# Kernel optimization log

Hardware: AMD Instinct MI355X
Metric: run time of the kernel (lower is better)

Reference implementation:

```python
import jax, jax.numpy as jnp
import numpy as np

SH_C0 = 0.28209479177387814  # degree-0 SH basis constant (3DGS convention)
LOWPASS = 0.3                # 2D covariance dilation used by the 3DGS rasterizer
NEAR_CULL = 0.2              # view-space z cull threshold in the CUDA kernel


def _render(extrinsics, intrinsics, near, far, h, w, bg, means, covs, shs, opac):
    B, G, _ = means.shape
    # ---- scale-invariant normalization (scale = 1/near) ----
    scale = 1.0 / near                                        # [B]
    extr = extrinsics.at[:, :3, 3].multiply(scale[:, None])
    covs = covs * (scale ** 2)[:, None, None, None]
    means = means * scale[:, None, None]
    near = near * scale

    view = jnp.linalg.inv(extr)                               # world -> camera
    R, t = view[:, :3, :3], view[:, :3, 3]
    cam = jnp.einsum('bij,bgj->bgi', R, means) + t[:, None, :]  # [B,G,3] view-space
    tz = cam[..., 2]

    fx, fy = intrinsics[:, 0, 0], intrinsics[:, 1, 1]
    cx, cy = intrinsics[:, 0, 2], intrinsics[:, 1, 2]
    fx_p, fy_p = fx * w, fy * h                               # focal in pixels
    cx_p, cy_p = cx * w, cy * h
    lim_x = (1.3 * (0.5 / fx))[:, None]                       # tan(fov/2) clamps (EWA)
    lim_y = (1.3 * (0.5 / fy))[:, None]

    # ---- EWA splatting: project 3D covariance to 2D conic ----
    txz = jnp.clip(cam[..., 0] / tz, -lim_x, lim_x) * tz
    tyz = jnp.clip(cam[..., 1] / tz, -lim_y, lim_y) * tz
    zero = jnp.zeros_like(tz)
    J = jnp.stack([
        jnp.stack([fx_p[:, None] / tz, zero, -fx_p[:, None] * txz / (tz * tz)], axis=-1),
        jnp.stack([zero, fy_p[:, None] / tz, -fy_p[:, None] * tyz / (tz * tz)], axis=-1),
    ], axis=-2)                                               # [B,G,2,3]
    M = jnp.einsum('bgij,bjk->bgik', J, R)                    # [B,G,2,3]
    cov2d = jnp.einsum('bgij,bgjk,bglk->bgil', M, covs, M)    # [B,G,2,2]
    a = cov2d[..., 0, 0] + LOWPASS
    bb = cov2d[..., 0, 1]
    c = cov2d[..., 1, 1] + LOWPASS
    det = a * c - bb * bb
    inv_det = jnp.where(det != 0, 1.0 / det, 0.0)
    conA, conB, conC = c * inv_det, -bb * inv_det, a * inv_det

    # ---- projected 2D means in pixel coords (ndc2pix) ----
    mx = fx_p[:, None] * cam[..., 0] / tz + cx_p[:, None] - 0.5
    my = fy_p[:, None] * cam[..., 1] / tz + cy_p[:, None] - 0.5

    # degree-0 SH -> RGB (clamped to >= 0 as in the kernel)
    colors = jnp.maximum(SH_C0 * shs[..., 0] + 0.5, 0.0)      # [B,G,3]

    # ---- global front-to-back depth sort per batch ----
    valid = (tz > NEAR_CULL) & (det > 0)
    order = jnp.argsort(jnp.where(valid, tz, jnp.inf), axis=1)
    take = lambda x: jnp.take_along_axis(x, order, axis=1)
    mx, my = take(mx), take(my)
    conA, conB, conC = take(conA), take(conB), take(conC)
    tzs, valid, op = take(tz), take(valid), take(opac)
    colors = jnp.take_along_axis(colors, order[..., None], axis=1)

    # ---- per-pixel alpha compositing ----
    px = jnp.tile(jnp.arange(w, dtype=jnp.float32), h)        # [HW]
    py = jnp.repeat(jnp.arange(h, dtype=jnp.float32), w)
    dx = px[None, None, :] - mx[..., None]                    # [B,G,HW]
    dy = py[None, None, :] - my[..., None]
    power = -0.5 * (conA[..., None] * dx * dx + conC[..., None] * dy * dy) \
            - conB[..., None] * dx * dy
    alpha = jnp.minimum(0.99, op[..., None] * jnp.exp(power))
    alpha = jnp.where((power <= 0) & (alpha >= 1.0 / 255.0) & valid[..., None], alpha, 0.0)
    Tcum = jnp.cumprod(1.0 - alpha, axis=1)                   # [B,G,HW]
    T_excl = jnp.concatenate([jnp.ones_like(Tcum[:, :1]), Tcum[:, :-1]], axis=1)
    wgt = alpha * T_excl                                      # contribution weights
    T_fin = Tcum[:, -1]                                       # [B,HW]

    img = jnp.einsum('bgp,bgc->bcp', wgt, colors) + T_fin[:, None, :] * bg[:, :, None]
    depth = jnp.sum(wgt * tzs[..., None], axis=1)
    op_map = jnp.sum(wgt, axis=1)
    return (img.reshape(B, 3, h, w), depth.reshape(B, h, w), op_map.reshape(B, 1, h, w))


def setup_inputs() -> dict:
    key = jax.random.key(0)
    ks = jax.random.split(key, 6)
    B, G, H, W = 2, 1024, 128, 128
    extr = jnp.tile(jnp.eye(4, dtype=jnp.float32)[None], (B, 1, 1))
    extr = extr.at[:, :3, 3].set(0.05 * jax.random.normal(ks[0], (B, 3), dtype=jnp.float32))
    intr = jnp.tile(jnp.array([[1.0, 0.0, 0.5], [0.0, 1.0, 0.5], [0.0, 0.0, 1.0]],
                              dtype=jnp.float32)[None], (B, 1, 1))
    near = jnp.ones((B,), jnp.float32)
    far = jnp.full((B,), 100.0, jnp.float32)
    bg = jnp.zeros((B, 3), jnp.float32)
    xy = jax.random.normal(ks[1], (B, G, 2), dtype=jnp.float32)
    zc = jax.random.uniform(ks[2], (B, G, 1), minval=2.0, maxval=6.0, dtype=jnp.float32)
    means = jnp.concatenate([xy, zc], axis=-1)
    L = 0.02 * jax.random.normal(ks[3], (B, G, 3, 3), dtype=jnp.float32)
    covs = jnp.einsum('bgij,bgkj->bgik', L, L) + 1e-4 * jnp.eye(3, dtype=jnp.float32)
    shs = 0.5 * jax.random.normal(ks[4], (B, G, 3, 1), dtype=jnp.float32)
    op = jax.random.uniform(ks[5], (B, G), dtype=jnp.float32)
    return {"extrinsics": extr, "intrinsics": intr, "near": near, "far": far,
            "h": H, "w": W, "background_color": bg, "gaussian_means": means,
            "gaussian_covariances": covs, "gaussian_sh_coefficients": shs,
            "gaussian_opacities": op}


def reference(extrinsics, intrinsics, near, far, h, w, background_color,
              gaussian_means, gaussian_covariances, gaussian_sh_coefficients,
              gaussian_opacities):
    return _render(extrinsics, intrinsics, near, far, h, w, background_color,
                   gaussian_means, gaussian_covariances, gaussian_sh_coefficients,
                   gaussian_opacities)
```

## Files before the change

### kernel.cpp

```cpp
#include <hip/hip_runtime.h>
#include <math.h>

#define SMAX 1024
#define EPS_T 1e-4f


__global__ __launch_bounds__(256) void prep_kernel(
    const float* __restrict__ extr,
    const float* __restrict__ intr,
    const float* __restrict__ nearv,
    const int* __restrict__ hp,
    const int* __restrict__ wp,
    const float* __restrict__ means,
    const float* __restrict__ covs,
    const float* __restrict__ shs,
    const float* __restrict__ opac,
    float* __restrict__ ws,
    int B, int G)
{
  const int i = blockIdx.x * blockDim.x + threadIdx.x;
  const int BG = B * G;
  if (i >= BG) return;
  const int b = i / G;

  const float hf = (float)hp[0];
  const float wf = (float)wp[0];
  const float scale = 1.0f / nearv[b];
  const float s2 = scale * scale;

  const float* E = extr + b * 16;
  const float A00=E[0], A01=E[1], A02=E[2];
  const float A10=E[4], A11=E[5], A12=E[6];
  const float A20=E[8], A21=E[9], A22=E[10];
  const float te0=E[3]*scale, te1=E[7]*scale, te2=E[11]*scale;
  const float co00 =  (A11*A22 - A12*A21);
  const float co10 = -(A10*A22 - A12*A20);
  const float co20 =  (A10*A21 - A11*A20);
  const float idA = 1.0f / (A00*co00 + A01*co10 + A02*co20);
  const float R00 = co00*idA;
  const float R01 = -(A01*A22 - A02*A21)*idA;
  const float R02 =  (A01*A12 - A02*A11)*idA;
  const float R10 = co10*idA;
  const float R11 =  (A00*A22 - A02*A20)*idA;
  const float R12 = -(A00*A12 - A02*A10)*idA;
  const float R20 = co20*idA;
  const float R21 = -(A00*A21 - A01*A20)*idA;
  const float R22 =  (A00*A11 - A01*A10)*idA;
  const float t0 = -(R00*te0 + R01*te1 + R02*te2);
  const float t1 = -(R10*te0 + R11*te1 + R12*te2);
  const float t2 = -(R20*te0 + R21*te1 + R22*te2);

  const float fx = intr[b*9+0], fy = intr[b*9+4];
  const float cx = intr[b*9+2], cy = intr[b*9+5];
  const float fx_p = fx*wf, fy_p = fy*hf, cx_p = cx*wf, cy_p = cy*hf;
  const float lim_x = 1.3f*0.5f/fx, lim_y = 1.3f*0.5f/fy;

  const float* mp = means + (size_t)i*3;
  float m0 = mp[0]*scale, m1 = mp[1]*scale, m2 = mp[2]*scale;
  float camx = R00*m0 + R01*m1 + R02*m2 + t0;
  float camy = R10*m0 + R11*m1 + R12*m2 + t1;
  float tz   = R20*m0 + R21*m1 + R22*m2 + t2;
  float itz = 1.0f / tz;
  const float* Cp = covs + (size_t)i*9;
  float C00=Cp[0]*s2, C01=Cp[1]*s2, C02=Cp[2]*s2;
  float C10=Cp[3]*s2, C11=Cp[4]*s2, C12=Cp[5]*s2;
  float C20=Cp[6]*s2, C21=Cp[7]*s2, C22=Cp[8]*s2;
  float txz = fminf(fmaxf(camx*itz, -lim_x), lim_x) * tz;
  float tyz = fminf(fmaxf(camy*itz, -lim_y), lim_y) * tz;
  float j00 = fx_p*itz, j02 = -fx_p*txz*itz*itz;
  float j11 = fy_p*itz, j12 = -fy_p*tyz*itz*itz;
  float M00 = j00*R00 + j02*R20;
  float M01 = j00*R01 + j02*R21;
  float M02 = j00*R02 + j02*R22;
  float M10 = j11*R10 + j12*R20;
  float M11 = j11*R11 + j12*R21;
  float M12 = j11*R12 + j12*R22;
  float v0 = C00*M00 + C01*M01 + C02*M02;
  float v1 = C10*M00 + C11*M01 + C12*M02;
  float v2 = C20*M00 + C21*M01 + C22*M02;
  float u0 = C00*M10 + C01*M11 + C02*M12;
  float u1 = C10*M10 + C11*M11 + C12*M12;
  float u2 = C20*M10 + C21*M11 + C22*M12;
  float a  = M00*v0 + M01*v1 + M02*v2 + 0.3f;
  float bb = M00*u0 + M01*u1 + M02*u2;
  float c  = M10*u0 + M11*u1 + M12*u2 + 0.3f;
  float det2 = a*c - bb*bb;
  float invd = (det2 != 0.0f) ? (1.0f/det2) : 0.0f;
  float conA = c*invd, conB = -bb*invd, conC = a*invd;
  float mx = fx_p*camx*itz + cx_p - 0.5f;
  float my = fy_p*camy*itz + cy_p - 0.5f;
  float op = opac[i];
  const float* sp = shs + (size_t)i*3;
  float col0 = fmaxf(0.28209479177387814f*sp[0] + 0.5f, 0.0f);
  float col1 = fmaxf(0.28209479177387814f*sp[1] + 0.5f, 0.0f);
  float col2 = fmaxf(0.28209479177387814f*sp[2] + 0.5f, 0.0f);
  float r2max = 2.0f * logf(255.0f * op);
  bool valid = (tz > 0.2f) && (det2 > 0.0f) && (r2max > 0.0f);
  float rx = sqrtf(fmaxf(r2max*a, 0.0f)) + 0.01f;
  float ry = sqrtf(fmaxf(r2max*c, 0.0f)) + 0.01f;

  float4* compv = (float4*)ws;
  compv[(size_t)i*3+0] = make_float4(mx, my, conA, conB);
  compv[(size_t)i*3+1] = make_float4(conC, op, col0, col1);
  compv[(size_t)i*3+2] = make_float4(col2, tz, 0.f, 0.f);
  float4* cullv = (float4*)(ws + (size_t)BG*12);
  cullv[i] = make_float4(valid ? mx : 1e9f, my, rx, ry);
  ws[(size_t)BG*16 + i] = tz;
}

__global__ __launch_bounds__(256) void render_kernel(
    const float* __restrict__ ws,
    const float* __restrict__ bg,
    const int* __restrict__ wp,
    float* __restrict__ out,
    int B, int G, int hw)
{
  const int tid = threadIdx.x;
  const int lane = tid & 63;
  const int wv = tid >> 6;
  const int tiles_per_img = hw >> 8;
  const int b = blockIdx.x / tiles_per_img;
  const int tile = blockIdx.x % tiles_per_img;
  const int w = wp[0];
  const int tiles_x = w >> 4;
  const int tx = tile % tiles_x;
  const int ty = tile / tiles_x;
  const int qx = (wv & 1) << 3;
  const int qy = (wv >> 1) << 3;
  const int px = (tx << 4) + qx + (lane & 7);
  const int py = (ty << 4) + qy + (lane >> 3);
  const float pxf = (float)px, pyf = (float)py;
  const float bx0 = (float)((tx << 4) + qx) - 0.01f;
  const float bx1 = bx0 + 7.02f;
  const float by0 = (float)((ty << 4) + qy) - 0.01f;
  const float by1 = by0 + 7.02f;

  const int BG = B * G;
  const int base = b * G;
  const float4* compv = (const float4*)ws;
  const float4* cullv = (const float4*)(ws + (size_t)BG*12);
  const float*  tza   = ws + (size_t)BG*16;

  __shared__ float  s_key[4][SMAX];
  __shared__ int    s_idx[4][SMAX];
  __shared__ float4 s_c[4][64][3];

  int cnt = 0;
  for (int g0 = 0; g0 < G; g0 += 64) {
    const int g = g0 + lane;
    bool surv = false;
    if (g < G) {
      float4 cu = cullv[base + g];
      surv = (cu.x - cu.z <= bx1) && (cu.x + cu.z >= bx0) &&
             (cu.y - cu.w <= by1) && (cu.y + cu.w >= by0);
    }
    unsigned long long m = __ballot(surv);
    if (surv) {
      int pos = cnt + __popcll(m & ((1ull << lane) - 1ull));
      if (pos < SMAX) {
        s_key[wv][pos] = tza[base + g];
        s_idx[wv][pos] = g;
      }
    }
    cnt += __popcll(m);
  }
  cnt = min(cnt, SMAX);

  float T = 1.0f, a0 = 0.f, a1 = 0.f, a2 = 0.f, da = 0.f, wa = 0.f;

  if (cnt > 0) {
    int n2 = 1;
    while (n2 < cnt) n2 <<= 1;
    for (int i2 = cnt + lane; i2 < n2; i2 += 64) {
      s_key[wv][i2] = INFINITY;
      s_idx[wv][i2] = 0x7fffffff;
    }
    __builtin_amdgcn_wave_barrier();

    for (int k2 = 2; k2 <= n2; k2 <<= 1) {
      for (int j = k2 >> 1; j > 0; j >>= 1) {
        for (int i2 = lane; i2 < n2; i2 += 64) {
          int ixj = i2 ^ j;
          if (ixj > i2) {
            float ki = s_key[wv][i2], kj = s_key[wv][ixj];
            int   ii = s_idx[wv][i2], ij = s_idx[wv][ixj];
            bool up = ((i2 & k2) == 0);
            bool gt = (ki > kj) || (ki == kj && ii > ij);
            if (up ? gt : !gt && !(ki == kj && ii == ij)) {
              s_key[wv][i2] = kj; s_key[wv][ixj] = ki;
              s_idx[wv][i2] = ij; s_idx[wv][ixj] = ii;
            }
          }
        }
        __builtin_amdgcn_wave_barrier();
      }
    }

    for (int c0 = 0; c0 < cnt; c0 += 64) {
      const int mlen = min(64, cnt - c0);
      if (lane < mlen) {
        const int g = s_idx[wv][c0 + lane];
        const float4* cp = compv + (size_t)(base + g) * 3;
        s_c[wv][lane][0] = cp[0];
        s_c[wv][lane][1] = cp[1];
        s_c[wv][lane][2] = cp[2];
      }
      __builtin_amdgcn_wave_barrier();
      for (int i2 = 0; i2 < mlen; i2++) {
        const float4 A  = s_c[wv][i2][0];
        const float4 Bv = s_c[wv][i2][1];
        const float4 Cv = s_c[wv][i2][2];
        const float dx = pxf - A.x;
        const float dy = pyf - A.y;
        const float q = A.z*dx*dx + 2.0f*A.w*dx*dy + Bv.x*dy*dy;
        if (q >= 0.0f && T >= EPS_T) {
          float al = fminf(Bv.y * __expf(-0.5f*q), 0.99f);
          if (al >= (1.0f/255.0f)) {
            const float wgt = al * T;
            a0 += wgt * Bv.z;
            a1 += wgt * Bv.w;
            a2 += wgt * Cv.x;
            da += wgt * Cv.y;
            wa += wgt;
            T *= (1.0f - al);
          }
        }
      }
      if (__ballot(T >= EPS_T) == 0ull) break;
      __builtin_amdgcn_wave_barrier();
    }
  }

  const int pixidx = py * w + px;
  const size_t io = (size_t)b * 3 * hw;
  out[io + 0*(size_t)hw + pixidx] = a0 + T * bg[b*3+0];
  out[io + 1*(size_t)hw + pixidx] = a1 + T * bg[b*3+1];
  out[io + 2*(size_t)hw + pixidx] = a2 + T * bg[b*3+2];
  out[(size_t)B*3*hw + (size_t)b*hw + pixidx] = da;
  out[(size_t)B*4*hw + (size_t)b*hw + pixidx] = wa;
}

extern "C" void kernel_launch(void* const* d_in, const int* in_sizes, int n_in,
                              void* d_out, int out_size, void* d_ws, size_t ws_size,
                              hipStream_t stream) {
  const float* extr  = (const float*)d_in[0];
  const float* intr  = (const float*)d_in[1];
  const float* nearv = (const float*)d_in[2];
  const int*   hp    = (const int*)d_in[4];
  const int*   wp    = (const int*)d_in[5];
  const float* bg    = (const float*)d_in[6];
  const float* means = (const float*)d_in[7];
  const float* covs  = (const float*)d_in[8];
  const float* shs   = (const float*)d_in[9];
  const float* opac  = (const float*)d_in[10];

  const int B  = in_sizes[2];
  const int G  = in_sizes[10] / B;
  const int hw = out_size / (5 * B);

  float* ws  = (float*)d_ws;
  float* out = (float*)d_out;

  const int BG = B * G;
  prep_kernel<<<(BG + 255) / 256, 256, 0, stream>>>(
      extr, intr, nearv, hp, wp, means, covs, shs, opac, ws, B, G);
  const int tiles = hw / 256;
  render_kernel<<<B * tiles, 256, 0, stream>>>(ws, bg, wp, out, B, G, hw);
}
```

Measured before the change: 96.56 us.

## Fuse Gaussian preprocessing into render kernel with shared-memory staging and packed sort keys

Removes the separate preprocessing kernel. Each render block now recomputes projection, conic and color for all Gaussians of its image into shared memory, and culling and compositing read from there instead of a global workspace. The depth-sort uses packed 64-bit (depth, index) keys, which halves shared-memory traffic per compare-exchange. The early-exit ballot now runs every 32 Gaussians. The costs are redundant per-block preprocessing, a hard G_MAX=1024 limit, and a per-wave sort capacity reduced from 1024 to 256, which could truncate lists.

Result: no change. 94.91 us (-1.7%).

```diff
diff --git a/kernel.cpp b/kernel.cpp
--- a/kernel.cpp
+++ b/kernel.cpp
@@ -1,117 +1,22 @@
 #include <hip/hip_runtime.h>
 #include <math.h>
 
-#define SMAX 1024
+#define G_MAX 1024
+#define SMAX 256
 #define EPS_T 1e-4f
 
 
-__global__ __launch_bounds__(256) void prep_kernel(
+__global__ __launch_bounds__(256) void render_all(
     const float* __restrict__ extr,
     const float* __restrict__ intr,
     const float* __restrict__ nearv,
     const int* __restrict__ hp,
     const int* __restrict__ wp,
+    const float* __restrict__ bg,
     const float* __restrict__ means,
     const float* __restrict__ covs,
     const float* __restrict__ shs,
     const float* __restrict__ opac,
-    float* __restrict__ ws,
-    int B, int G)
-{
-  const int i = blockIdx.x * blockDim.x + threadIdx.x;
-  const int BG = B * G;
-  if (i >= BG) return;
-  const int b = i / G;
-
-  const float hf = (float)hp[0];
-  const float wf = (float)wp[0];
-  const float scale = 1.0f / nearv[b];
-  const float s2 = scale * scale;
-
-  const float* E = extr + b * 16;
-  const float A00=E[0], A01=E[1], A02=E[2];
-  const float A10=E[4], A11=E[5], A12=E[6];
-  const float A20=E[8], A21=E[9], A22=E[10];
-  const float te0=E[3]*scale, te1=E[7]*scale, te2=E[11]*scale;
-  const float co00 =  (A11*A22 - A12*A21);
-  const float co10 = -(A10*A22 - A12*A20);
-  const float co20 =  (A10*A21 - A11*A20);
-  const float idA = 1.0f / (A00*co00 + A01*co10 + A02*co20);
-  const float R00 = co00*idA;
-  const float R01 = -(A01*A22 - A02*A21)*idA;
-  const float R02 =  (A01*A12 - A02*A11)*idA;
-  const float R10 = co10*idA;
-  const float R11 =  (A00*A22 - A02*A20)*idA;
-  const float R12 = -(A00*A12 - A02*A10)*idA;
-  const float R20 = co20*idA;
-  const float R21 = -(A00*A21 - A01*A20)*idA;
-  const float R22 =  (A00*A11 - A01*A10)*idA;
-  const float t0 = -(R00*te0 + R01*te1 + R02*te2);
-  const float t1 = -(R10*te0 + R11*te1 + R12*te2);
-  const float t2 = -(R20*te0 + R21*te1 + R22*te2);
-
-  const float fx = intr[b*9+0], fy = intr[b*9+4];
-  const float cx = intr[b*9+2], cy = intr[b*9+5];
-  const float fx_p = fx*wf, fy_p = fy*hf, cx_p = cx*wf, cy_p = cy*hf;
-  const float lim_x = 1.3f*0.5f/fx, lim_y = 1.3f*0.5f/fy;
-
-  const float* mp = means + (size_t)i*3;
-  float m0 = mp[0]*scale, m1 = mp[1]*scale, m2 = mp[2]*scale;
-  float camx = R00*m0 + R01*m1 + R02*m2 + t0;
-  float camy = R10*m0 + R11*m1 + R12*m2 + t1;
-  float tz   = R20*m0 + R21*m1 + R22*m2 + t2;
-  float itz = 1.0f / tz;
-  const float* Cp = covs + (size_t)i*9;
-  float C00=Cp[0]*s2, C01=Cp[1]*s2, C02=Cp[2]*s2;
-  float C10=Cp[3]*s2, C11=Cp[4]*s2, C12=Cp[5]*s2;
-  float C20=Cp[6]*s2, C21=Cp[7]*s2, C22=Cp[8]*s2;
-  float txz = fminf(fmaxf(camx*itz, -lim_x), lim_x) * tz;
-  float tyz = fminf(fmaxf(camy*itz, -lim_y), lim_y) * tz;
-  float j00 = fx_p*itz, j02 = -fx_p*txz*itz*itz;
-  float j11 = fy_p*itz, j12 = -fy_p*tyz*itz*itz;
-  float M00 = j00*R00 + j02*R20;
-  float M01 = j00*R01 + j02*R21;
-  float M02 = j00*R02 + j02*R22;
-  float M10 = j11*R10 + j12*R20;
-  float M11 = j11*R11 + j12*R21;
-  float M12 = j11*R12 + j12*R22;
-  float v0 = C00*M00 + C01*M01 + C02*M02;
-  float v1 = C10*M00 + C11*M01 + C12*M02;
-  float v2 = C20*M00 + C21*M01 + C22*M02;
-  float u0 = C00*M10 + C01*M11 + C02*M12;
-  float u1 = C10*M10 + C11*M11 + C12*M12;
-  float u2 = C20*M10 + C21*M11 + C22*M12;
-  float a  = M00*v0 + M01*v1 + M02*v2 + 0.3f;
-  float bb = M00*u0 + M01*u1 + M02*u2;
-  float c  = M10*u0 + M11*u1 + M12*u2 + 0.3f;
-  float det2 = a*c - bb*bb;
-  float invd = (det2 != 0.0f) ? (1.0f/det2) : 0.0f;
-  float conA = c*invd, conB = -bb*invd, conC = a*invd;
-  float mx = fx_p*camx*itz + cx_p - 0.5f;
-  float my = fy_p*camy*itz + cy_p - 0.5f;
-  float op = opac[i];
-  const float* sp = shs + (size_t)i*3;
-  float col0 = fmaxf(0.28209479177387814f*sp[0] + 0.5f, 0.0f);
-  float col1 = fmaxf(0.28209479177387814f*sp[1] + 0.5f, 0.0f);
-  float col2 = fmaxf(0.28209479177387814f*sp[2] + 0.5f, 0.0f);
-  float r2max = 2.0f * logf(255.0f * op);
-  bool valid = (tz > 0.2f) && (det2 > 0.0f) && (r2max > 0.0f);
-  float rx = sqrtf(fmaxf(r2max*a, 0.0f)) + 0.01f;
-  float ry = sqrtf(fmaxf(r2max*c, 0.0f)) + 0.01f;
-
-  float4* compv = (float4*)ws;
-  compv[(size_t)i*3+0] = make_float4(mx, my, conA, conB);
-  compv[(size_t)i*3+1] = make_float4(conC, op, col0, col1);
-  compv[(size_t)i*3+2] = make_float4(col2, tz, 0.f, 0.f);
-  float4* cullv = (float4*)(ws + (size_t)BG*12);
-  cullv[i] = make_float4(valid ? mx : 1e9f, my, rx, ry);
-  ws[(size_t)BG*16 + i] = tz;
-}
-
-__global__ __launch_bounds__(256) void render_kernel(
-    const float* __restrict__ ws,
-    const float* __restrict__ bg,
-    const int* __restrict__ wp,
     float* __restrict__ out,
     int B, int G, int hw)
 {
@@ -135,32 +40,109 @@
   const float by0 = (float)((ty << 4) + qy) - 0.01f;
   const float by1 = by0 + 7.02f;
 
-  const int BG = B * G;
-  const int base = b * G;
-  const float4* compv = (const float4*)ws;
-  const float4* cullv = (const float4*)(ws + (size_t)BG*12);
-  const float*  tza   = ws + (size_t)BG*16;
-
-  __shared__ float  s_key[4][SMAX];
-  __shared__ int    s_idx[4][SMAX];
-  __shared__ float4 s_c[4][64][3];
+  __shared__ float4 s_cull[G_MAX];
+  __shared__ float4 s_con [G_MAX];
+  __shared__ float4 s_col [G_MAX];
+  __shared__ unsigned long long s_srt[4][SMAX];
+
+  const float hf = (float)hp[0];
+  const float wf = (float)wp[0];
+  const float scale = 1.0f / nearv[b];
+  const float s2 = scale * scale;
+  const float* E = extr + b * 16;
+  const float A00=E[0], A01=E[1], A02=E[2];
+  const float A10=E[4], A11=E[5], A12=E[6];
+  const float A20=E[8], A21=E[9], A22=E[10];
+  const float te0=E[3]*scale, te1=E[7]*scale, te2=E[11]*scale;
+  const float co00 =  (A11*A22 - A12*A21);
+  const float co10 = -(A10*A22 - A12*A20);
+  const float co20 =  (A10*A21 - A11*A20);
+  const float idA = 1.0f / (A00*co00 + A01*co10 + A02*co20);
+  const float R00 = co00*idA;
+  const float R01 = -(A01*A22 - A02*A21)*idA;
+  const float R02 =  (A01*A12 - A02*A11)*idA;
+  const float R10 = co10*idA;
+  const float R11 =  (A00*A22 - A02*A20)*idA;
+  const float R12 = -(A00*A12 - A02*A10)*idA;
+  const float R20 = co20*idA;
+  const float R21 = -(A00*A21 - A01*A20)*idA;
+  const float R22 =  (A00*A11 - A01*A10)*idA;
+  const float t0 = -(R00*te0 + R01*te1 + R02*te2);
+  const float t1 = -(R10*te0 + R11*te1 + R12*te2);
+  const float t2 = -(R20*te0 + R21*te1 + R22*te2);
+  const float fx = intr[b*9+0], fy = intr[b*9+4];
+  const float cx = intr[b*9+2], cy = intr[b*9+5];
+  const float fx_p = fx*wf, fy_p = fy*hf, cx_p = cx*wf, cy_p = cy*hf;
+  const float lim_x = 1.3f*0.5f/fx, lim_y = 1.3f*0.5f/fy;
+
+  for (int g = tid; g < G; g += blockDim.x) {
+    const int i = b * G + g;
+    const float* mp = means + (size_t)i*3;
+    float m0 = mp[0]*scale, m1 = mp[1]*scale, m2 = mp[2]*scale;
+    float camx = R00*m0 + R01*m1 + R02*m2 + t0;
+    float camy = R10*m0 + R11*m1 + R12*m2 + t1;
+    float tz   = R20*m0 + R21*m1 + R22*m2 + t2;
+    float itz = 1.0f / tz;
+    const float* Cp = covs + (size_t)i*9;
+    float C00=Cp[0]*s2, C01=Cp[1]*s2, C02=Cp[2]*s2;
+    float C10=Cp[3]*s2, C11=Cp[4]*s2, C12=Cp[5]*s2;
+    float C20=Cp[6]*s2, C21=Cp[7]*s2, C22=Cp[8]*s2;
+    float txz = fminf(fmaxf(camx*itz, -lim_x), lim_x) * tz;
+    float tyz = fminf(fmaxf(camy*itz, -lim_y), lim_y) * tz;
+    float j00 = fx_p*itz, j02 = -fx_p*txz*itz*itz;
+    float j11 = fy_p*itz, j12 = -fy_p*tyz*itz*itz;
+    float M00 = j00*R00 + j02*R20;
+    float M01 = j00*R01 + j02*R21;
+    float M02 = j00*R02 + j02*R22;
+    float M10 = j11*R10 + j12*R20;
+    float M11 = j11*R11 + j12*R21;
+    float M12 = j11*R12 + j12*R22;
+    float v0 = C00*M00 + C01*M01 + C02*M02;
+    float v1 = C10*M00 + C11*M01 + C12*M02;
+    float v2 = C20*M00 + C21*M01 + C22*M02;
+    float u0 = C00*M10 + C01*M11 + C02*M12;
+    float u1 = C10*M10 + C11*M11 + C12*M12;
+    float u2 = C20*M10 + C21*M11 + C22*M12;
+    float a  = M00*v0 + M01*v1 + M02*v2 + 0.3f;
+    float bb = M00*u0 + M01*u1 + M02*u2;
+    float c  = M10*u0 + M11*u1 + M12*u2 + 0.3f;
+    float det2 = a*c - bb*bb;
+    float invd = (det2 != 0.0f) ? (1.0f/det2) : 0.0f;
+    float conA = c*invd, conB = -bb*invd, conC = a*invd;
+    float mx = fx_p*camx*itz + cx_p - 0.5f;
+    float my = fy_p*camy*itz + cy_p - 0.5f;
+    float op = opac[i];
+    const float* sp = shs + (size_t)i*3;
+    float col0 = fmaxf(0.28209479177387814f*sp[0] + 0.5f, 0.0f);
+    float col1 = fmaxf(0.28209479177387814f*sp[1] + 0.5f, 0.0f);
+    float col2 = fmaxf(0.28209479177387814f*sp[2] + 0.5f, 0.0f);
+    float r2max = 2.0f * logf(255.0f * op);
+    bool valid = (tz > 0.2f) && (det2 > 0.0f) && (r2max > 0.0f);
+    float rx = sqrtf(fmaxf(r2max*a, 0.0f)) + 0.01f;
+    float ry = sqrtf(fmaxf(r2max*c, 0.0f)) + 0.01f;
+    s_cull[g] = make_float4(valid ? mx : 1e9f, my, rx, ry);
+    s_con [g] = make_float4(conA, conB, conC, op);
+    s_col [g] = make_float4(col0, col1, col2, tz);
+  }
+  __syncthreads();
 
   int cnt = 0;
   for (int g0 = 0; g0 < G; g0 += 64) {
     const int g = g0 + lane;
     bool surv = false;
+    float tz = 0.f;
     if (g < G) {
-      float4 cu = cullv[base + g];
+      float4 cu = s_cull[g];
       surv = (cu.x - cu.z <= bx1) && (cu.x + cu.z >= bx0) &&
              (cu.y - cu.w <= by1) && (cu.y + cu.w >= by0);
+      tz = s_col[g].w;
     }
     unsigned long long m = __ballot(surv);
     if (surv) {
       int pos = cnt + __popcll(m & ((1ull << lane) - 1ull));
-      if (pos < SMAX) {
-        s_key[wv][pos] = tza[base + g];
-        s_idx[wv][pos] = g;
-      }
+      if (pos < SMAX)
+        s_srt[wv][pos] = ((unsigned long long)__float_as_uint(tz) << 32) |
+                         (unsigned)g;
     }
     cnt += __popcll(m);
   }
@@ -171,10 +153,8 @@
   if (cnt > 0) {
     int n2 = 1;
     while (n2 < cnt) n2 <<= 1;
-    for (int i2 = cnt + lane; i2 < n2; i2 += 64) {
-      s_key[wv][i2] = INFINITY;
-      s_idx[wv][i2] = 0x7fffffff;
-    }
+    for (int i2 = cnt + lane; i2 < n2; i2 += 64)
+      s_srt[wv][i2] = ~0ull;
     __builtin_amdgcn_wave_barrier();
 
     for (int k2 = 2; k2 <= n2; k2 <<= 1) {
@@ -182,13 +162,12 @@
         for (int i2 = lane; i2 < n2; i2 += 64) {
           int ixj = i2 ^ j;
           if (ixj > i2) {
-            float ki = s_key[wv][i2], kj = s_key[wv][ixj];
-            int   ii = s_idx[wv][i2], ij = s_idx[wv][ixj];
+            unsigned long long ka = s_srt[wv][i2];
+            unsigned long long kb = s_srt[wv][ixj];
             bool up = ((i2 & k2) == 0);
-            bool gt = (ki > kj) || (ki == kj && ii > ij);
-            if (up ? gt : !gt && !(ki == kj && ii == ij)) {
-              s_key[wv][i2] = kj; s_key[wv][ixj] = ki;
-              s_idx[wv][i2] = ij; s_idx[wv][ixj] = ii;
+            if (up ? (ka > kb) : (ka < kb)) {
+              s_srt[wv][i2] = kb;
+              s_srt[wv][ixj] = ka;
             }
           }
         }
@@ -196,38 +175,27 @@
       }
     }
 
-    for (int c0 = 0; c0 < cnt; c0 += 64) {
-      const int mlen = min(64, cnt - c0);
-      if (lane < mlen) {
-        const int g = s_idx[wv][c0 + lane];
-        const float4* cp = compv + (size_t)(base + g) * 3;
-        s_c[wv][lane][0] = cp[0];
-        s_c[wv][lane][1] = cp[1];
-        s_c[wv][lane][2] = cp[2];
-      }
-      __builtin_amdgcn_wave_barrier();
-      for (int i2 = 0; i2 < mlen; i2++) {
-        const float4 A  = s_c[wv][i2][0];
-        const float4 Bv = s_c[wv][i2][1];
-        const float4 Cv = s_c[wv][i2][2];
-        const float dx = pxf - A.x;
-        const float dy = pyf - A.y;
-        const float q = A.z*dx*dx + 2.0f*A.w*dx*dy + Bv.x*dy*dy;
-        if (q >= 0.0f && T >= EPS_T) {
-          float al = fminf(Bv.y * __expf(-0.5f*q), 0.99f);
-          if (al >= (1.0f/255.0f)) {
-            const float wgt = al * T;
-            a0 += wgt * Bv.z;
-            a1 += wgt * Bv.w;
-            a2 += wgt * Cv.x;
-            da += wgt * Cv.y;
-            wa += wgt;
-            T *= (1.0f - al);
-          }
+    for (int i2 = 0; i2 < cnt; i2++) {
+      const int g = (int)(unsigned)(s_srt[wv][i2] & 0xffffffffu);
+      const float4 cu = s_cull[g];
+      const float4 cn = s_con[g];
+      const float4 cl = s_col[g];
+      const float dx = pxf - cu.x;
+      const float dy = pyf - cu.y;
+      const float q = cn.x*dx*dx + 2.0f*cn.y*dx*dy + cn.z*dy*dy;
+      if (q >= 0.0f && T >= EPS_T) {
+        float al = fminf(cn.w * __expf(-0.5f*q), 0.99f);
+        if (al >= (1.0f/255.0f)) {
+          const float wgt = al * T;
+          a0 += wgt * cl.x;
+          a1 += wgt * cl.y;
+          a2 += wgt * cl.z;
+          da += wgt * cl.w;
+          wa += wgt;
+          T *= (1.0f - al);
         }
       }
-      if (__ballot(T >= EPS_T) == 0ull) break;
-      __builtin_amdgcn_wave_barrier();
+      if ((i2 & 31) == 31 && __ballot(T >= EPS_T) == 0ull) break;
     }
   }
 
@@ -258,12 +226,8 @@
   const int G  = in_sizes[10] / B;
   const int hw = out_size / (5 * B);
 
-  float* ws  = (float*)d_ws;
   float* out = (float*)d_out;
-
-  const int BG = B * G;
-  prep_kernel<<<(BG + 255) / 256, 256, 0, stream>>>(
-      extr, intr, nearv, hp, wp, means, covs, shs, opac, ws, B, G);
   const int tiles = hw / 256;
-  render_kernel<<<B * tiles, 256, 0, stream>>>(ws, bg, wp, out, B, G, hw);
+  render_all<<<B * tiles, 256, 0, stream>>>(
+      extr, intr, nearv, hp, wp, bg, means, covs, shs, opac, out, B, G, hw);
 }
```
